# Performance work log

Hardware: AMD Instinct MI355X
Metric: run time of the kernel (lower is better)

Reference implementation:

```python
import jax, jax.numpy as jnp
import numpy as np

BN_EPS = 1e-3


def _knn_group(p1, p2, k):
    # p1, p2: [N, 3]. For each point in p1 find k nearest in p2.
    d2 = (jnp.sum(p1 * p1, -1)[:, None] + jnp.sum(p2 * p2, -1)[None, :]
          - 2.0 * (p1 @ p2.T))                      # [N, N]
    _, idx = jax.lax.top_k(-d2, k)                   # [N, k]
    nn = p2[idx]                                     # [N, k, 3]
    resi = nn - p1[:, None, :]                       # [N, k, 3]
    dist = jnp.linalg.norm(resi, axis=-1, keepdims=True)
    feat = jnp.concatenate([resi, dist], axis=-1)    # [N, k, 4]
    return feat, nn


def _conv_bn_relu(x, W, b, g, be):
    # x: [B, Cin, N, K]; 1x1 conv == channel matmul, BN uses batch stats (train mode)
    y = jnp.einsum('oi,binK->bonK', W, x) + b[None, :, None, None]
    m = jnp.mean(y, axis=(0, 2, 3), keepdims=True)
    v = jnp.var(y, axis=(0, 2, 3), keepdims=True)
    y = g[None, :, None, None] * (y - m) * jax.lax.rsqrt(v + BN_EPS) + be[None, :, None, None]
    return jax.nn.relu(y)


def setup_inputs() -> dict:
    key = jax.random.key(0)
    ks = jax.random.split(key, 8)
    B, N, k = 4, 4096, 32
    C = [4, 64, 64, 128]
    inp = {
        'points1': jax.random.normal(ks[0], (B, 3, N), jnp.float32),
        'points2': jax.random.normal(ks[1], (B, 3, N), jnp.float32),
        'k': k,
        't': jax.random.uniform(ks[2], (B,), jnp.float32),
    }
    for i in range(3):
        kw = jax.random.fold_in(ks[3], i)
        inp[f'W{i+1}'] = jax.random.normal(kw, (C[i + 1], C[i]), jnp.float32) * (1.0 / np.sqrt(C[i]))
        inp[f'b{i+1}'] = jnp.zeros((C[i + 1],), jnp.float32)
        inp[f'g{i+1}'] = jnp.ones((C[i + 1],), jnp.float32)
        inp[f'be{i+1}'] = jnp.zeros((C[i + 1],), jnp.float32)
    return inp


def reference(points1, points2, k, t, W1, b1, g1, be1, W2, b2, g2, be2, W3, b3, g3, be3):
    p1 = jnp.transpose(points1, (0, 2, 1))           # [B, N, 3]
    p2 = jnp.transpose(points2, (0, 2, 1))
    knn = jax.vmap(_knn_group, in_axes=(0, 0, None))
    f1, nn1 = knn(p1, p1, k)                          # [B, N, k, 4], [B, N, k, 3]
    f2, nn2 = knn(p1, p2, k)
    feats = jnp.concatenate([f1, f2], axis=2)         # [B, N, 2k, 4]
    grouped = jnp.concatenate([nn1, nn2], axis=2)     # [B, N, 2k, 3]
    x = jnp.transpose(feats, (0, 3, 1, 2))            # [B, 4, N, 2k]
    x = _conv_bn_relu(x, W1, b1, g1, be1)
    x = _conv_bn_relu(x, W2, b2, g2, be2)
    x = _conv_bn_relu(x, W3, b3, g3, be3)             # [B, 128, N, 2k]
    scores = jnp.max(x, axis=1)                       # [B, N, 2k]
    w = jax.nn.softmax(scores, axis=-1)               # [B, N, 2k]
    fused = jnp.einsum('bnk,bnkc->bcn', w, grouped)   # [B, 3, N]
    return fused
```

## Files before the change

kernel.cpp:

```cpp
#include <hip/hip_runtime.h>
#include <hip/hip_bf16.h>

#define B_   4
#define N_   4096
#define KNN_ 32
#define KK_  64
#define MTOT 1048576
#define BN_EPS 1e-3f

typedef unsigned int u32;
typedef unsigned long long u64;
typedef __attribute__((ext_vector_type(8))) short bf16x8;
typedef __attribute__((ext_vector_type(4))) float f32x4;

__device__ __forceinline__ ushort f2bf_bits(float f) {
    u32 b = __float_as_uint(f);
    b += 0x7fffu + ((b >> 16) & 1u);
    return (ushort)(b >> 16);
}

__device__ __forceinline__ float med3f(float a, float b, float c) {
    return __builtin_amdgcn_fmed3f(a, b, c);
}

__device__ __forceinline__ float rank_e3(float cx, float cy, float2 zw,
                                         float m2x, float m2y, float m2z) {
    return fmaf(m2x, cx, fmaf(m2y, cy, fmaf(m2z, zw.x, zw.y)));
}

__device__ __forceinline__ u32 ordkey(float f) {
    u32 u = __float_as_uint(f);
    return u ^ (u32)(((int)u >> 31) | 0x80000000);
}
__device__ __forceinline__ float ordinv(u32 k) {
    u32 u = (k & 0x80000000u) ? (k ^ 0x80000000u) : ~k;
    return __uint_as_float(u);
}

__global__ __launch_bounds__(512, 2) void knn_kernel(
    const float* __restrict__ p1, const float* __restrict__ p2,
    float* __restrict__ feats, float* __restrict__ mom)
{
    __shared__ float2 cxy[N_];
    __shared__ float2 czw[N_];

    const int tid  = threadIdx.x;
    const int wave = tid >> 6, lane = tid & 63;
    const int pb    = blockIdx.x >> 6;
    const int chunk = blockIdx.x & 63;
    const int pr = pb >> 2, b = pb & 3;
    const int start = chunk * 64;

    const float* srcb = (pr ? p2 : p1) + (size_t)b * 3 * N_;
    for (int n = tid; n < N_; n += 512) {
        float x = srcb[n], y = srcb[N_ + n], z = srcb[2*N_ + n];
        cxy[n] = make_float2(x, y);
        czw[n] = make_float2(z, fmaf(x, x, fmaf(y, y, z * z)));
    }
    __syncthreads();

    const float* p1b = p1 + (size_t)b * 3 * N_;
    const u64 below = (1ull << lane) - 1ull;
    const float FMAX = 3.402823466e+38f;

    for (int n = start + wave; n < start + 64; n += 8) {
        float qx, qy, qz;
        if (pr == 0) { float2 q = cxy[n]; qx = q.x; qy = q.y; qz = czw[n].x; }
        else         { qx = p1b[n]; qy = p1b[N_ + n]; qz = p1b[2*N_ + n]; }
        const float m2x = -2.0f * qx, m2y = -2.0f * qy, m2z = -2.0f * qz;

        float keys[64];
        float A0 = FMAX, A1 = FMAX, A2 = FMAX, A3 = FMAX;
        float B0 = FMAX, B1 = FMAX, B2 = FMAX, B3 = FMAX;
        #pragma unroll
        for (int j = 0; j < 32; ++j) {
            {
                float2 c  = cxy[j * 64 + lane];
                float2 zw = czw[j * 64 + lane];
                float  e  = rank_e3(c.x, c.y, zw, m2x, m2y, m2z);
                keys[j] = e;
                A3 = med3f(e, A2, A3);
                A2 = med3f(e, A1, A2);
                A1 = med3f(e, A0, A1);
                A0 = fminf(A0, e);
            }
            {
                float2 c  = cxy[(j + 32) * 64 + lane];
                float2 zw = czw[(j + 32) * 64 + lane];
                float  e  = rank_e3(c.x, c.y, zw, m2x, m2y, m2z);
                keys[j + 32] = e;
                B3 = med3f(e, B2, B3);
                B2 = med3f(e, B1, B2);
                B1 = med3f(e, B0, B1);
                B0 = fminf(B0, e);
            }
        }
        #pragma unroll
        for (int m = 0; m < 4; ++m) {
            float x = (m == 0) ? B0 : (m == 1) ? B1 : (m == 2) ? B2 : B3;
            A3 = med3f(x, A2, A3);
            A2 = med3f(x, A1, A2);
            A1 = med3f(x, A0, A1);
            A0 = fminf(A0, x);
        }
        u32 k0 = ordkey(A0), k1 = ordkey(A1), k2 = ordkey(A2), k3 = ordkey(A3);

        u32 mn = k0, mx = k3;
        #pragma unroll
        for (int off = 1; off < 64; off <<= 1) {
            mn = min(mn, (u32)__shfl_xor((int)mn, off, 64));
            mx = max(mx, (u32)__shfl_xor((int)mx, off, 64));
        }
        u32 lo = mn, hi = mx;
        while (lo < hi) {
            u32 mid = lo + ((hi - lo) >> 1);
            int c = __popcll(__ballot(k0 <= mid)) + __popcll(__ballot(k1 <= mid))
                  + __popcll(__ballot(k2 <= mid)) + __popcll(__ballot(k3 <= mid));
            if (c >= 32) hi = mid; else lo = mid + 1;
        }
        u32 T = lo;
        float Tf = ordinv(T);

        int nl;
        if (__ballot(A3 <= Tf) == 0ull) {
            nl = __popcll(__ballot(A0 < Tf)) + __popcll(__ballot(A1 < Tf))
               + __popcll(__ballot(A2 < Tf)) + __popcll(__ballot(A3 < Tf));
        } else {
            nl = 0;
            #pragma unroll
            for (int j = 0; j < 64; ++j) nl += __popcll(__ballot(keys[j] < Tf));
            if (nl > 31) {
                u32 lo2 = 0u, hi2 = T;
                while (lo2 < hi2) {
                    u32 mid = lo2 + ((hi2 - lo2) >> 1);
                    float mf = ordinv(mid);
                    int c = 0;
                    #pragma unroll
                    for (int j = 0; j < 64; ++j) c += __popcll(__ballot(keys[j] <= mf));
                    if (c >= 32) hi2 = mid; else lo2 = mid + 1;
                }
                T = lo2;
                Tf = ordinv(T);
                nl = 0;
                #pragma unroll
                for (int j = 0; j < 64; ++j) nl += __popcll(__ballot(keys[j] < Tf));
            }
        }
        const int need_eq = 32 - nl;

        float* fout = feats + ((size_t)(b * N_ + n) * KK_ + pr * KNN_) * 4;
        int base = 0, eq_seen = 0;
        #pragma unroll
        for (int j = 0; j < 64; ++j) {
            float e = keys[j];
            bool lt = e < Tf;
            bool eq = e == Tf;
            u64 mlt = __ballot(lt);
            u64 meq = __ballot(eq);
            if (mlt | meq) {
                int slot = -1;
                if (lt) slot = base + __popcll(mlt & below);
                else if (eq) {
                    int es = eq_seen + __popcll(meq & below);
                    if (es < need_eq) slot = nl + es;
                }
                if (slot >= 0) {
                    float2 c  = cxy[j * 64 + lane];
                    float2 zw = czw[j * 64 + lane];
                    float rx = c.x - qx, ry = c.y - qy, rz = zw.x - qz;
                    float dist = sqrtf(fmaf(rx, rx, fmaf(ry, ry, rz*rz)));
                    *(float4*)(fout + slot * 4) = make_float4(rx, ry, rz, dist);
                }
                base    += __popcll(mlt);
                eq_seen += __popcll(meq);
            }
        }
    }

    __syncthreads();
    float mm[14];
    #pragma unroll
    for (int s = 0; s < 14; ++s) mm[s] = 0.f;
    const float4* fb = (const float4*)feats
                     + ((size_t)(b * N_ + start) * KK_ + pr * KNN_);
    for (int idx = tid; idx < 64 * 32; idx += 512) {
        int row = idx >> 5, col = idx & 31;
        float4 f = fb[(size_t)row * KK_ + col];
        float rx = f.x, ry = f.y, rz = f.z, dist = f.w;
        mm[0] += rx; mm[1] += ry; mm[2] += rz; mm[3] += dist;
        mm[4]  = fmaf(rx, rx, mm[4]);   mm[5]  = fmaf(rx, ry, mm[5]);
        mm[6]  = fmaf(rx, rz, mm[6]);   mm[7]  = fmaf(rx, dist, mm[7]);
        mm[8]  = fmaf(ry, ry, mm[8]);   mm[9]  = fmaf(ry, rz, mm[9]);
        mm[10] = fmaf(ry, dist, mm[10]); mm[11] = fmaf(rz, rz, mm[11]);
        mm[12] = fmaf(rz, dist, mm[12]); mm[13] = fmaf(dist, dist, mm[13]);
    }
    #pragma unroll
    for (int s = 0; s < 14; ++s) {
        #pragma unroll
        for (int off = 1; off < 64; off <<= 1) mm[s] += __shfl_xor(mm[s], off, 64);
    }
    float* partf = (float*)cxy;
    if (lane == 0) {
        #pragma unroll
        for (int s = 0; s < 14; ++s) partf[wave * 14 + s] = mm[s];
    }
    __syncthreads();
    if (tid < 14) {
        float v = 0.f;
        #pragma unroll
        for (int w8 = 0; w8 < 8; ++w8) v += partf[w8 * 14 + tid];
        atomicAdd(&mom[tid * 16], v);
    }
}

__global__ __launch_bounds__(256) void conv2_mfma(
    const float* __restrict__ feats,
    const float* __restrict__ W1,
    const float* __restrict__ g1, const float* __restrict__ be1,
    const float* __restrict__ W2,
    const float* __restrict__ mom,
    ushort* __restrict__ y2F, float* __restrict__ s2S, float* __restrict__ s2Q)
{
    __shared__ float statS[64], statQ[64];
    const int tid = threadIdx.x;
    const int wid = tid >> 6, l = tid & 63, q = l >> 4, i = l & 15;
    if (tid < 64) { statS[tid] = 0.f; statQ[tid] = 0.f; }

    const float invM = 1.0f / MTOT;
    const float M0 = mom[0*16], M1 = mom[1*16], M2 = mom[2*16], M3 = mom[3*16];
    const float Sxx = mom[4*16],  Sxy = mom[5*16],  Sxz = mom[6*16],  Sxd = mom[7*16];
    const float Syy = mom[8*16],  Syz = mom[9*16],  Syd = mom[10*16];
    const float Szz = mom[11*16], Szd = mom[12*16], Sdd = mom[13*16];

    float4 w1f[16];
    float  c1v[16];
    #pragma unroll
    for (int h = 0; h < 2; ++h)
      #pragma unroll
      for (int j = 0; j < 8; ++j) {
        int ci = h*32 + q*8 + j;
        float w0 = W1[ci*4+0], w1 = W1[ci*4+1], w2 = W1[ci*4+2], w3 = W1[ci*4+3];
        float meanf = (w0*M0 + w1*M1 + w2*M2 + w3*M3) * invM;
        float qq = w0*(w0*Sxx + 2.f*(w1*Sxy + w2*Sxz + w3*Sxd))
                 + w1*(w1*Syy + 2.f*(w2*Syz + w3*Syd))
                 + w2*(w2*Szz + 2.f*w3*Szd)
                 + w3*w3*Sdd;
        float var = qq * invM - meanf * meanf;
        float sc  = g1[ci] * rsqrtf(var + BN_EPS);
        w1f[h*8+j] = make_float4(sc*w0, sc*w1, sc*w2, sc*w3);
        c1v[h*8+j] = fmaf(-sc, meanf, be1[ci]);
      }
    bf16x8 a2[4][2];
    #pragma unroll
    for (int t = 0; t < 4; ++t)
      #pragma unroll
      for (int h = 0; h < 2; ++h)
        #pragma unroll
        for (int j = 0; j < 8; ++j)
          a2[t][h][j] = (short)f2bf_bits(W2[(t*16 + i)*64 + h*32 + q*8 + j]);

    float ssum[16], ssq[16];
    #pragma unroll
    for (int s = 0; s < 16; ++s) { ssum[s] = 0.f; ssq[s] = 0.f; }
    __syncthreads();

    for (int r16 = 0; r16 < 16; ++r16) {
        const int row = blockIdx.x * 16 + r16;
        float4 f = ((const float4*)feats)[row*64 + wid*16 + i];
        bf16x8 xb[2];
        #pragma unroll
        for (int h = 0; h < 2; ++h)
          #pragma unroll
          for (int j = 0; j < 8; ++j) {
            float4 w = w1f[h*8+j];
            float x = fmaxf(fmaf(w.x, f.x, fmaf(w.y, f.y, fmaf(w.z, f.z, fmaf(w.w, f.w, c1v[h*8+j])))), 0.f);
            xb[h][j] = (short)f2bf_bits(x);
          }
        f32x4 acc[4];
        #pragma unroll
        for (int t = 0; t < 4; ++t) acc[t] = (f32x4){0.f,0.f,0.f,0.f};
        #pragma unroll
        for (int t = 0; t < 4; ++t) {
            acc[t] = __builtin_amdgcn_mfma_f32_16x16x32_bf16(a2[t][0], xb[0], acc[t], 0, 0, 0);
            acc[t] = __builtin_amdgcn_mfma_f32_16x16x32_bf16(a2[t][1], xb[1], acc[t], 0, 0, 0);
        }
        ushort* wp = y2F + row*4096 + wid*1024 + q*64 + i*4;
        #pragma unroll
        for (int t = 0; t < 4; ++t) {
            #pragma unroll
            for (int reg = 0; reg < 4; ++reg) {
                float y = acc[t][reg];
                ssum[t*4+reg] += y;
                ssq[t*4+reg]  = fmaf(y, y, ssq[t*4+reg]);
            }
            uint2 pk;
            pk.x = (u32)f2bf_bits(acc[t][0]) | ((u32)f2bf_bits(acc[t][1]) << 16);
            pk.y = (u32)f2bf_bits(acc[t][2]) | ((u32)f2bf_bits(acc[t][3]) << 16);
            *(uint2*)(wp + t*256) = pk;
        }
    }
    #pragma unroll
    for (int s = 0; s < 16; ++s) {
        #pragma unroll
        for (int off = 1; off < 16; off <<= 1) {
            ssum[s] += __shfl_xor(ssum[s], off, 64);
            ssq[s]  += __shfl_xor(ssq[s],  off, 64);
        }
    }
    if (i == 0) {
        #pragma unroll
        for (int s = 0; s < 16; ++s) {
            int co = (s >> 2)*16 + q*4 + (s & 3);
            atomicAdd(&statS[co], ssum[s]);
            atomicAdd(&statQ[co], ssq[s]);
        }
    }
    __syncthreads();
    if (tid < 64) { atomicAdd(&s2S[tid], statS[tid]); atomicAdd(&s2Q[tid], statQ[tid]); }
}

__global__ __launch_bounds__(256) void conv3_stats(
    ushort* __restrict__ y2F,
    const float* __restrict__ g2, const float* __restrict__ be2,
    const float* __restrict__ W3,
    const float* __restrict__ s2S, const float* __restrict__ s2Q,
    float* __restrict__ s3S, float* __restrict__ s3Q)
{
    __shared__ float statS[128], statQ[128];
    const int tid = threadIdx.x;
    const int w = tid >> 6, l = tid & 63, q = l >> 4, i = l & 15;
    const int ph = w >> 1, oh = w & 1;
    if (tid < 128) { statS[tid] = 0.f; statQ[tid] = 0.f; }

    float sc2v[16], sh2v[16];
    #pragma unroll
    for (int h = 0; h < 2; ++h)
      #pragma unroll
      for (int j = 0; j < 8; ++j) {
        int ci = h*32 + q*8 + j;
        float m  = s2S[ci] * (1.0f / MTOT);
        float v  = s2Q[ci] * (1.0f / MTOT) - m * m;
        float sc = g2[ci] * rsqrtf(v + BN_EPS);
        sc2v[h*8+j] = sc;
        sh2v[h*8+j] = fmaf(-sc, m, be2[ci]);
      }
    bf16x8 a3[4][2];
    #pragma unroll
    for (int t = 0; t < 4; ++t)
      #pragma unroll
      for (int h = 0; h < 2; ++h)
        #pragma unroll
        for (int j = 0; j < 8; ++j)
          a3[t][h][j] = (short)f2bf_bits(W3[((oh*4 + t)*16 + i)*64 + h*32 + q*8 + j]);

    float ssum[16], ssq[16];
    #pragma unroll
    for (int s = 0; s < 16; ++s) { ssum[s] = 0.f; ssq[s] = 0.f; }

    for (int r16 = 0; r16 < 16; ++r16) {
        const int row = blockIdx.x * 16 + r16;
        ushort* rp0 = y2F + row*4096 + (2*ph)*1024 + q*128 + i*4;
        ushort* rp1 = rp0 + 1024;
        uint2 a00 = *(const uint2*)(rp0);       uint2 a01 = *(const uint2*)(rp0 + 64);
        uint2 a10 = *(const uint2*)(rp0 + 512); uint2 a11 = *(const uint2*)(rp0 + 576);
        uint2 b00 = *(const uint2*)(rp1);       uint2 b01 = *(const uint2*)(rp1 + 64);
        uint2 b10 = *(const uint2*)(rp1 + 512); uint2 b11 = *(const uint2*)(rp1 + 576);

        bf16x8 xa[2], xc[2];
        #pragma unroll
        for (int pt2 = 0; pt2 < 2; ++pt2) {
            uint2 v00 = pt2 ? b00 : a00, v01 = pt2 ? b01 : a01;
            uint2 v10 = pt2 ? b10 : a10, v11 = pt2 ? b11 : a11;
            bf16x8* dst = pt2 ? xc : xa;
            #pragma unroll
            for (int h = 0; h < 2; ++h) {
                u32 w0 = h ? v10.x : v00.x, w1 = h ? v10.y : v00.y;
                u32 w2 = h ? v11.x : v01.x, w3 = h ? v11.y : v01.y;
                float xf[8];
                xf[0] = __uint_as_float(w0 << 16); xf[1] = __uint_as_float(w0 & 0xffff0000u);
                xf[2] = __uint_as_float(w1 << 16); xf[3] = __uint_as_float(w1 & 0xffff0000u);
                xf[4] = __uint_as_float(w2 << 16); xf[5] = __uint_as_float(w2 & 0xffff0000u);
                xf[6] = __uint_as_float(w3 << 16); xf[7] = __uint_as_float(w3 & 0xffff0000u);
                #pragma unroll
                for (int j = 0; j < 8; ++j) {
                    float x = fmaxf(fmaf(sc2v[h*8+j], xf[j], sh2v[h*8+j]), 0.f);
                    dst[h][j] = (short)f2bf_bits(x);
                }
            }
        }
        __syncthreads();
        if (oh == 0) {
            uint4 ua0 = *(uint4*)&xa[0], ua1 = *(uint4*)&xa[1];
            uint4 uc0 = *(uint4*)&xc[0], uc1 = *(uint4*)&xc[1];
            *(uint2*)(rp0)       = make_uint2(ua0.x, ua0.y);
            *(uint2*)(rp0 + 64)  = make_uint2(ua0.z, ua0.w);
            *(uint2*)(rp0 + 512) = make_uint2(ua1.x, ua1.y);
            *(uint2*)(rp0 + 576) = make_uint2(ua1.z, ua1.w);
            *(uint2*)(rp1)       = make_uint2(uc0.x, uc0.y);
            *(uint2*)(rp1 + 64)  = make_uint2(uc0.z, uc0.w);
            *(uint2*)(rp1 + 512) = make_uint2(uc1.x, uc1.y);
            *(uint2*)(rp1 + 576) = make_uint2(uc1.z, uc1.w);
        }
        #pragma unroll
        for (int t = 0; t < 4; ++t) {
            f32x4 A = (f32x4){0.f,0.f,0.f,0.f};
            A = __builtin_amdgcn_mfma_f32_16x16x32_bf16(a3[t][0], xa[0], A, 0, 0, 0);
            A = __builtin_amdgcn_mfma_f32_16x16x32_bf16(a3[t][1], xa[1], A, 0, 0, 0);
            f32x4 Bv = (f32x4){0.f,0.f,0.f,0.f};
            Bv = __builtin_amdgcn_mfma_f32_16x16x32_bf16(a3[t][0], xc[0], Bv, 0, 0, 0);
            Bv = __builtin_amdgcn_mfma_f32_16x16x32_bf16(a3[t][1], xc[1], Bv, 0, 0, 0);
            #pragma unroll
            for (int reg = 0; reg < 4; ++reg) {
                float ya = A[reg], yb = Bv[reg];
                ssum[t*4+reg] += ya + yb;
                ssq[t*4+reg]  = fmaf(ya, ya, fmaf(yb, yb, ssq[t*4+reg]));
            }
        }
    }
    #pragma unroll
    for (int s = 0; s < 16; ++s) {
        #pragma unroll
        for (int off = 1; off < 16; off <<= 1) {
            ssum[s] += __shfl_xor(ssum[s], off, 64);
            ssq[s]  += __shfl_xor(ssq[s],  off, 64);
        }
    }
    if (i == 0) {
        #pragma unroll
        for (int s = 0; s < 16; ++s) {
            int co = oh*64 + (s >> 2)*16 + q*4 + (s & 3);
            atomicAdd(&statS[co], ssum[s]);
            atomicAdd(&statQ[co], ssq[s]);
        }
    }
    __syncthreads();
    if (tid < 128) { atomicAdd(&s3S[tid], statS[tid]); atomicAdd(&s3Q[tid], statQ[tid]); }
}

__global__ __launch_bounds__(256) void conv3_final(
    const ushort* __restrict__ x3F,
    const float* __restrict__ W3,
    const float* __restrict__ g3, const float* __restrict__ be3,
    const float* __restrict__ s3S, const float* __restrict__ s3Q,
    const float4* __restrict__ feats4, const float* __restrict__ p1,
    float* __restrict__ outp)
{
    __shared__ float sc3L[128], sh3L[128];
    __shared__ float s2L[2][2][64];
    const int tid = threadIdx.x;
    const int w = tid >> 6, l = tid & 63, q = l >> 4, i = l & 15;
    const int ph = w >> 1, oh = w & 1;

    if (tid < 128) {
        float m  = s3S[tid] * (1.0f / MTOT);
        float v  = s3Q[tid] * (1.0f / MTOT) - m * m;
        float sc = g3[tid] * rsqrtf(v + BN_EPS);
        sc3L[tid] = sc;
        sh3L[tid] = fmaf(-sc, m, be3[tid]);
    }
    bf16x8 a3[4][2];
    #pragma unroll
    for (int t = 0; t < 4; ++t)
      #pragma unroll
      for (int h = 0; h < 2; ++h)
        #pragma unroll
        for (int j = 0; j < 8; ++j)
          a3[t][h][j] = (short)f2bf_bits(W3[((oh*4 + t)*16 + i)*64 + h*32 + q*8 + j]);
    __syncthreads();

    for (int r16 = 0; r16 < 16; ++r16) {
        const int row = blockIdx.x * 16 + r16;
        #pragma unroll
        for (int pt2 = 0; pt2 < 2; ++pt2) {
            const int pt = 2*ph + pt2;
            const ushort* rp = x3F + row*4096 + pt*1024 + q*128 + i*4;
            uint2 u00 = *(const uint2*)(rp);       uint2 u01 = *(const uint2*)(rp + 64);
            uint2 u10 = *(const uint2*)(rp + 512); uint2 u11 = *(const uint2*)(rp + 576);
            uint4 v0 = make_uint4(u00.x, u00.y, u01.x, u01.y);
            uint4 v1 = make_uint4(u10.x, u10.y, u11.x, u11.y);
            bf16x8 xb0 = *(bf16x8*)&v0, xb1 = *(bf16x8*)&v1;
            float mx = -3.4e38f;
            #pragma unroll
            for (int t = 0; t < 4; ++t) {
                f32x4 a = (f32x4){0.f,0.f,0.f,0.f};
                a = __builtin_amdgcn_mfma_f32_16x16x32_bf16(a3[t][0], xb0, a, 0, 0, 0);
                a = __builtin_amdgcn_mfma_f32_16x16x32_bf16(a3[t][1], xb1, a, 0, 0, 0);
                const int co = oh*64 + t*16 + q*4;
                float4 s4 = *(const float4*)&sc3L[co];
                float4 h4 = *(const float4*)&sh3L[co];
                mx = fmaxf(mx, fmaf(s4.x, a[0], h4.x));
                mx = fmaxf(mx, fmaf(s4.y, a[1], h4.y));
                mx = fmaxf(mx, fmaf(s4.z, a[2], h4.z));
                mx = fmaxf(mx, fmaf(s4.w, a[3], h4.w));
            }
            mx = fmaxf(mx, __shfl_xor(mx, 16, 64));
            mx = fmaxf(mx, __shfl_xor(mx, 32, 64));
            if (q == 0) s2L[r16 & 1][oh][pt*16 + i] = mx;
        }
        __syncthreads();
        if (w == 0) {
            float sc = fmaxf(fmaxf(s2L[r16 & 1][0][l], s2L[r16 & 1][1][l]), 0.f);
            float m2 = sc;
            #pragma unroll
            for (int off = 1; off < 64; off <<= 1) m2 = fmaxf(m2, __shfl_xor(m2, off, 64));
            float e = __expf(sc - m2);
            float se = e;
            #pragma unroll
            for (int off = 1; off < 64; off <<= 1) se += __shfl_xor(se, off, 64);
            float wgt = e / se;
            const int bb = row >> 12, n = row & 4095;
            float qx = p1[(size_t)bb*3*N_ + n];
            float qy = p1[(size_t)bb*3*N_ + N_ + n];
            float qz = p1[(size_t)bb*3*N_ + 2*N_ + n];
            float4 f4 = feats4[row*64 + l];
            float ox = wgt * (f4.x + qx), oy = wgt * (f4.y + qy), oz = wgt * (f4.z + qz);
            #pragma unroll
            for (int off = 1; off < 64; off <<= 1) {
                ox += __shfl_xor(ox, off, 64);
                oy += __shfl_xor(oy, off, 64);
                oz += __shfl_xor(oz, off, 64);
            }
            if (l == 0) {
                outp[bb*3*N_ + 0*N_ + n] = ox;
                outp[bb*3*N_ + 1*N_ + n] = oy;
                outp[bb*3*N_ + 2*N_ + n] = oz;
            }
        }
    }
}

extern "C" void kernel_launch(void* const* d_in, const int* in_sizes, int n_in,
                              void* d_out, int out_size, void* d_ws, size_t ws_size,
                              hipStream_t stream)
{
    const float* p1  = (const float*)d_in[0];
    const float* p2  = (const float*)d_in[1];
    const float* W1  = (const float*)d_in[4];
    const float* g1  = (const float*)d_in[6];
    const float* be1 = (const float*)d_in[7];
    const float* W2  = (const float*)d_in[8];
    const float* g2  = (const float*)d_in[10];
    const float* be2 = (const float*)d_in[11];
    const float* W3  = (const float*)d_in[12];
    const float* g3  = (const float*)d_in[14];
    const float* be3 = (const float*)d_in[15];

    char* ws = (char*)d_ws;
    const size_t OFF_FEATS = 4096;
    const size_t OFF_Y2    = OFF_FEATS + (size_t)MTOT * 4 * 4;
    const size_t NEEDED    = OFF_Y2 + (size_t)MTOT * 64 * 2;
    if (ws_size < NEEDED) return;

    float* s2S = (float*)(ws + 512);  float* s2Q = (float*)(ws + 768);
    float* s3S = (float*)(ws + 1024); float* s3Q = (float*)(ws + 1536);
    float* mom = (float*)(ws + 2048);
    float* feats = (float*)(ws + OFF_FEATS);
    ushort* y2F  = (ushort*)(ws + OFF_Y2);

    hipMemsetAsync(ws, 0, 4096, stream);

    knn_kernel<<<512, 512, 0, stream>>>(p1, p2, feats, mom);
    conv2_mfma<<<1024, 256, 0, stream>>>(feats, W1, g1, be1, W2, mom,
                                         y2F, s2S, s2Q);
    conv3_stats<<<1024, 256, 0, stream>>>(y2F, g2, be2, W3,
                                          s2S, s2Q, s3S, s3Q);
    conv3_final<<<1024, 256, 0, stream>>>(y2F, W3, g3, be3, s3S, s3Q,
                                          (const float4*)feats, p1,
                                          (float*)d_out);
}
```

Baseline: 419.9 us.

## Recompute conv1/conv2 activations per pass instead of materializing y2 in global memory

Removes the 128 MB bf16 y2 intermediate buffer. Each of the conv3 stats and final kernels now recomputes conv1 and conv2 from the 16-byte feats rows and stages the BN2-ReLU output in shared memory, where it feeds the conv3 MFMAs. This trades a global write plus two reads (and an in-place rewrite) for extra MFMA and VALU work and more barriers per row.

```diff
diff --git a/kernel.cpp b/kernel.cpp
--- a/kernel.cpp
+++ b/kernel.cpp
@@ -213,13 +213,13 @@
     }
 }
 
-__global__ __launch_bounds__(256) void conv2_mfma(
+__global__ __launch_bounds__(256) void conv2_stats(
     const float* __restrict__ feats,
     const float* __restrict__ W1,
     const float* __restrict__ g1, const float* __restrict__ be1,
     const float* __restrict__ W2,
     const float* __restrict__ mom,
-    ushort* __restrict__ y2F, float* __restrict__ s2S, float* __restrict__ s2Q)
+    float* __restrict__ s2S, float* __restrict__ s2Q)
 {
     __shared__ float statS[64], statQ[64];
     const int tid = threadIdx.x;
@@ -284,20 +284,14 @@
             acc[t] = __builtin_amdgcn_mfma_f32_16x16x32_bf16(a2[t][0], xb[0], acc[t], 0, 0, 0);
             acc[t] = __builtin_amdgcn_mfma_f32_16x16x32_bf16(a2[t][1], xb[1], acc[t], 0, 0, 0);
         }
-        ushort* wp = y2F + row*4096 + wid*1024 + q*64 + i*4;
-        #pragma unroll
-        for (int t = 0; t < 4; ++t) {
-            #pragma unroll
-            for (int reg = 0; reg < 4; ++reg) {
-                float y = acc[t][reg];
-                ssum[t*4+reg] += y;
-                ssq[t*4+reg]  = fmaf(y, y, ssq[t*4+reg]);
-            }
-            uint2 pk;
-            pk.x = (u32)f2bf_bits(acc[t][0]) | ((u32)f2bf_bits(acc[t][1]) << 16);
-            pk.y = (u32)f2bf_bits(acc[t][2]) | ((u32)f2bf_bits(acc[t][3]) << 16);
-            *(uint2*)(wp + t*256) = pk;
-        }
+        #pragma unroll
+        for (int t = 0; t < 4; ++t)
+          #pragma unroll
+          for (int reg = 0; reg < 4; ++reg) {
+            float y = acc[t][reg];
+            ssum[t*4+reg] += y;
+            ssq[t*4+reg]  = fmaf(y, y, ssq[t*4+reg]);
+          }
     }
     #pragma unroll
     for (int s = 0; s < 16; ++s) {
@@ -319,96 +313,126 @@
     if (tid < 64) { atomicAdd(&s2S[tid], statS[tid]); atomicAdd(&s2Q[tid], statQ[tid]); }
 }
 
-__global__ __launch_bounds__(256) void conv3_stats(
-    ushort* __restrict__ y2F,
+
+__global__ __launch_bounds__(256) void conv3_stats_f(
+    const float* __restrict__ feats,
+    const float* __restrict__ W1,
+    const float* __restrict__ g1, const float* __restrict__ be1,
+    const float* __restrict__ W2,
+    const float* __restrict__ mom,
     const float* __restrict__ g2, const float* __restrict__ be2,
     const float* __restrict__ W3,
     const float* __restrict__ s2S, const float* __restrict__ s2Q,
     float* __restrict__ s3S, float* __restrict__ s3Q)
 {
-    __shared__ float statS[128], statQ[128];
+    __shared__ ushort x3L[4096];
+    __shared__ float  statS[128], statQ[128];
+    __shared__ float4 w1L[64];
+    __shared__ float  c1L[64], sc2L[64], sh2L[64];
+
     const int tid = threadIdx.x;
     const int w = tid >> 6, l = tid & 63, q = l >> 4, i = l & 15;
-    const int ph = w >> 1, oh = w & 1;
+    const int ph = w >> 1, oh = w & 1, wid = w;
     if (tid < 128) { statS[tid] = 0.f; statQ[tid] = 0.f; }
 
-    float sc2v[16], sh2v[16];
-    #pragma unroll
-    for (int h = 0; h < 2; ++h)
-      #pragma unroll
-      for (int j = 0; j < 8; ++j) {
-        int ci = h*32 + q*8 + j;
-        float m  = s2S[ci] * (1.0f / MTOT);
-        float v  = s2Q[ci] * (1.0f / MTOT) - m * m;
-        float sc = g2[ci] * rsqrtf(v + BN_EPS);
-        sc2v[h*8+j] = sc;
-        sh2v[h*8+j] = fmaf(-sc, m, be2[ci]);
-      }
-    bf16x8 a3[4][2];
+    if (tid < 64) {
+        const int ci = tid;
+        const float invM = 1.0f / MTOT;
+        float M0 = mom[0*16], M1 = mom[1*16], M2 = mom[2*16], M3 = mom[3*16];
+        float Sxx = mom[4*16],  Sxy = mom[5*16],  Sxz = mom[6*16],  Sxd = mom[7*16];
+        float Syy = mom[8*16],  Syz = mom[9*16],  Syd = mom[10*16];
+        float Szz = mom[11*16], Szd = mom[12*16], Sdd = mom[13*16];
+        float w0 = W1[ci*4+0], w1 = W1[ci*4+1], w2 = W1[ci*4+2], w3 = W1[ci*4+3];
+        float meanf = (w0*M0 + w1*M1 + w2*M2 + w3*M3) * invM;
+        float qq = w0*(w0*Sxx + 2.f*(w1*Sxy + w2*Sxz + w3*Sxd))
+                 + w1*(w1*Syy + 2.f*(w2*Syz + w3*Syd))
+                 + w2*(w2*Szz + 2.f*w3*Szd)
+                 + w3*w3*Sdd;
+        float var = qq * invM - meanf * meanf;
+        float sc  = g1[ci] * rsqrtf(var + BN_EPS);
+        w1L[ci] = make_float4(sc*w0, sc*w1, sc*w2, sc*w3);
+        c1L[ci] = fmaf(-sc, meanf, be1[ci]);
+        float m2  = s2S[ci] * invM;
+        float v2  = s2Q[ci] * invM - m2 * m2;
+        float sc2 = g2[ci] * rsqrtf(v2 + BN_EPS);
+        sc2L[ci] = sc2;
+        sh2L[ci] = fmaf(-sc2, m2, be2[ci]);
+    }
+
+    bf16x8 a2[4][2], a3[4][2];
     #pragma unroll
     for (int t = 0; t < 4; ++t)
       #pragma unroll
       for (int h = 0; h < 2; ++h)
         #pragma unroll
-        for (int j = 0; j < 8; ++j)
+        for (int j = 0; j < 8; ++j) {
+          a2[t][h][j] = (short)f2bf_bits(W2[(t*16 + i)*64 + h*32 + q*8 + j]);
           a3[t][h][j] = (short)f2bf_bits(W3[((oh*4 + t)*16 + i)*64 + h*32 + q*8 + j]);
+        }
 
     float ssum[16], ssq[16];
     #pragma unroll
     for (int s = 0; s < 16; ++s) { ssum[s] = 0.f; ssq[s] = 0.f; }
+    __syncthreads();
 
     for (int r16 = 0; r16 < 16; ++r16) {
         const int row = blockIdx.x * 16 + r16;
-        ushort* rp0 = y2F + row*4096 + (2*ph)*1024 + q*128 + i*4;
-        ushort* rp1 = rp0 + 1024;
+        float4 f = ((const float4*)feats)[row*64 + wid*16 + i];
+        bf16x8 xb[2];
+        #pragma unroll
+        for (int h = 0; h < 2; ++h)
+          #pragma unroll
+          for (int j = 0; j < 8; ++j) {
+            float4 wv = w1L[h*32 + q*8 + j];
+            float c1 = c1L[h*32 + q*8 + j];
+            float x = fmaxf(fmaf(wv.x, f.x, fmaf(wv.y, f.y, fmaf(wv.z, f.z, fmaf(wv.w, f.w, c1)))), 0.f);
+            xb[h][j] = (short)f2bf_bits(x);
+          }
+        f32x4 acc[4];
+        #pragma unroll
+        for (int t = 0; t < 4; ++t) acc[t] = (f32x4){0.f,0.f,0.f,0.f};
+        #pragma unroll
+        for (int t = 0; t < 4; ++t) {
+            acc[t] = __builtin_amdgcn_mfma_f32_16x16x32_bf16(a2[t][0], xb[0], acc[t], 0, 0, 0);
+            acc[t] = __builtin_amdgcn_mfma_f32_16x16x32_bf16(a2[t][1], xb[1], acc[t], 0, 0, 0);
+        }
+        #pragma unroll
+        for (int t = 0; t < 4; ++t) {
+            ushort o[4];
+            #pragma unroll
+            for (int reg = 0; reg < 4; ++reg) {
+                ushort yb = f2bf_bits(acc[t][reg]);
+                float xf = __uint_as_float(((u32)yb) << 16);
+                float x3 = fmaxf(fmaf(sc2L[t*16 + q*4 + reg], xf, sh2L[t*16 + q*4 + reg]), 0.f);
+                o[reg] = f2bf_bits(x3);
+            }
+            uint2 pk;
+            pk.x = (u32)o[0] | ((u32)o[1] << 16);
+            pk.y = (u32)o[2] | ((u32)o[3] << 16);
+            *(uint2*)&x3L[wid*1024 + t*256 + q*64 + i*4] = pk;
+        }
+        __syncthreads();
+
+        const ushort* rp0 = x3L + (2*ph)*1024 + q*128 + i*4;
+        const ushort* rp1 = rp0 + 1024;
         uint2 a00 = *(const uint2*)(rp0);       uint2 a01 = *(const uint2*)(rp0 + 64);
         uint2 a10 = *(const uint2*)(rp0 + 512); uint2 a11 = *(const uint2*)(rp0 + 576);
         uint2 b00 = *(const uint2*)(rp1);       uint2 b01 = *(const uint2*)(rp1 + 64);
         uint2 b10 = *(const uint2*)(rp1 + 512); uint2 b11 = *(const uint2*)(rp1 + 576);
-
-        bf16x8 xa[2], xc[2];
-        #pragma unroll
-        for (int pt2 = 0; pt2 < 2; ++pt2) {
-            uint2 v00 = pt2 ? b00 : a00, v01 = pt2 ? b01 : a01;
-            uint2 v10 = pt2 ? b10 : a10, v11 = pt2 ? b11 : a11;
-            bf16x8* dst = pt2 ? xc : xa;
-            #pragma unroll
-            for (int h = 0; h < 2; ++h) {
-                u32 w0 = h ? v10.x : v00.x, w1 = h ? v10.y : v00.y;
-                u32 w2 = h ? v11.x : v01.x, w3 = h ? v11.y : v01.y;
-                float xf[8];
-                xf[0] = __uint_as_float(w0 << 16); xf[1] = __uint_as_float(w0 & 0xffff0000u);
-                xf[2] = __uint_as_float(w1 << 16); xf[3] = __uint_as_float(w1 & 0xffff0000u);
-                xf[4] = __uint_as_float(w2 << 16); xf[5] = __uint_as_float(w2 & 0xffff0000u);
-                xf[6] = __uint_as_float(w3 << 16); xf[7] = __uint_as_float(w3 & 0xffff0000u);
-                #pragma unroll
-                for (int j = 0; j < 8; ++j) {
-                    float x = fmaxf(fmaf(sc2v[h*8+j], xf[j], sh2v[h*8+j]), 0.f);
-                    dst[h][j] = (short)f2bf_bits(x);
-                }
-            }
-        }
-        __syncthreads();
-        if (oh == 0) {
-            uint4 ua0 = *(uint4*)&xa[0], ua1 = *(uint4*)&xa[1];
-            uint4 uc0 = *(uint4*)&xc[0], uc1 = *(uint4*)&xc[1];
-            *(uint2*)(rp0)       = make_uint2(ua0.x, ua0.y);
-            *(uint2*)(rp0 + 64)  = make_uint2(ua0.z, ua0.w);
-            *(uint2*)(rp0 + 512) = make_uint2(ua1.x, ua1.y);
-            *(uint2*)(rp0 + 576) = make_uint2(ua1.z, ua1.w);
-            *(uint2*)(rp1)       = make_uint2(uc0.x, uc0.y);
-            *(uint2*)(rp1 + 64)  = make_uint2(uc0.z, uc0.w);
-            *(uint2*)(rp1 + 512) = make_uint2(uc1.x, uc1.y);
-            *(uint2*)(rp1 + 576) = make_uint2(uc1.z, uc1.w);
-        }
+        uint4 va0 = make_uint4(a00.x, a00.y, a01.x, a01.y);
+        uint4 va1 = make_uint4(a10.x, a10.y, a11.x, a11.y);
+        uint4 vc0 = make_uint4(b00.x, b00.y, b01.x, b01.y);
+        uint4 vc1 = make_uint4(b10.x, b10.y, b11.x, b11.y);
+        bf16x8 xa0 = *(bf16x8*)&va0, xa1 = *(bf16x8*)&va1;
+        bf16x8 xc0 = *(bf16x8*)&vc0, xc1 = *(bf16x8*)&vc1;
         #pragma unroll
         for (int t = 0; t < 4; ++t) {
             f32x4 A = (f32x4){0.f,0.f,0.f,0.f};
-            A = __builtin_amdgcn_mfma_f32_16x16x32_bf16(a3[t][0], xa[0], A, 0, 0, 0);
-            A = __builtin_amdgcn_mfma_f32_16x16x32_bf16(a3[t][1], xa[1], A, 0, 0, 0);
+            A = __builtin_amdgcn_mfma_f32_16x16x32_bf16(a3[t][0], xa0, A, 0, 0, 0);
+            A = __builtin_amdgcn_mfma_f32_16x16x32_bf16(a3[t][1], xa1, A, 0, 0, 0);
             f32x4 Bv = (f32x4){0.f,0.f,0.f,0.f};
-            Bv = __builtin_amdgcn_mfma_f32_16x16x32_bf16(a3[t][0], xc[0], Bv, 0, 0, 0);
-            Bv = __builtin_amdgcn_mfma_f32_16x16x32_bf16(a3[t][1], xc[1], Bv, 0, 0, 0);
+            Bv = __builtin_amdgcn_mfma_f32_16x16x32_bf16(a3[t][0], xc0, Bv, 0, 0, 0);
+            Bv = __builtin_amdgcn_mfma_f32_16x16x32_bf16(a3[t][1], xc1, Bv, 0, 0, 0);
             #pragma unroll
             for (int reg = 0; reg < 4; ++reg) {
                 float ya = A[reg], yb = Bv[reg];
@@ -416,6 +440,7 @@
                 ssq[t*4+reg]  = fmaf(ya, ya, fmaf(yb, yb, ssq[t*4+reg]));
             }
         }
+        __syncthreads();
     }
     #pragma unroll
     for (int s = 0; s < 16; ++s) {
@@ -437,43 +462,115 @@
     if (tid < 128) { atomicAdd(&s3S[tid], statS[tid]); atomicAdd(&s3Q[tid], statQ[tid]); }
 }
 
-__global__ __launch_bounds__(256) void conv3_final(
-    const ushort* __restrict__ x3F,
+__global__ __launch_bounds__(256) void conv3_final_f(
+    const float* __restrict__ feats,
+    const float* __restrict__ W1,
+    const float* __restrict__ g1, const float* __restrict__ be1,
+    const float* __restrict__ W2,
+    const float* __restrict__ mom,
+    const float* __restrict__ g2, const float* __restrict__ be2,
     const float* __restrict__ W3,
+    const float* __restrict__ s2S, const float* __restrict__ s2Q,
     const float* __restrict__ g3, const float* __restrict__ be3,
     const float* __restrict__ s3S, const float* __restrict__ s3Q,
-    const float4* __restrict__ feats4, const float* __restrict__ p1,
-    float* __restrict__ outp)
+    const float* __restrict__ p1, float* __restrict__ outp)
 {
-    __shared__ float sc3L[128], sh3L[128];
-    __shared__ float s2L[2][2][64];
+    __shared__ ushort x3L[4096];
+    __shared__ float4 w1L[64];
+    __shared__ float  c1L[64], sc2L[64], sh2L[64];
+    __shared__ float  sc3L[128], sh3L[128];
+    __shared__ float  s2L[2][2][64];
+
     const int tid = threadIdx.x;
     const int w = tid >> 6, l = tid & 63, q = l >> 4, i = l & 15;
-    const int ph = w >> 1, oh = w & 1;
-
+    const int ph = w >> 1, oh = w & 1, wid = w;
+
+    if (tid < 64) {
+        const int ci = tid;
+        const float invM = 1.0f / MTOT;
+        float M0 = mom[0*16], M1 = mom[1*16], M2 = mom[2*16], M3 = mom[3*16];
+        float Sxx = mom[4*16],  Sxy = mom[5*16],  Sxz = mom[6*16],  Sxd = mom[7*16];
+        float Syy = mom[8*16],  Syz = mom[9*16],  Syd = mom[10*16];
+        float Szz = mom[11*16], Szd = mom[12*16], Sdd = mom[13*16];
+        float w0 = W1[ci*4+0], w1 = W1[ci*4+1], w2 = W1[ci*4+2], w3 = W1[ci*4+3];
+        float meanf = (w0*M0 + w1*M1 + w2*M2 + w3*M3) * invM;
+        float qq = w0*(w0*Sxx + 2.f*(w1*Sxy + w2*Sxz + w3*Sxd))
+                 + w1*(w1*Syy + 2.f*(w2*Syz + w3*Syd))
+                 + w2*(w2*Szz + 2.f*w3*Szd)
+                 + w3*w3*Sdd;
+        float var = qq * invM - meanf * meanf;
+        float sc  = g1[ci] * rsqrtf(var + BN_EPS);
+        w1L[ci] = make_float4(sc*w0, sc*w1, sc*w2, sc*w3);
+        c1L[ci] = fmaf(-sc, meanf, be1[ci]);
+        float m2  = s2S[ci] * invM;
+        float v2  = s2Q[ci] * invM - m2 * m2;
+        float sc2 = g2[ci] * rsqrtf(v2 + BN_EPS);
+        sc2L[ci] = sc2;
+        sh2L[ci] = fmaf(-sc2, m2, be2[ci]);
+    }
     if (tid < 128) {
-        float m  = s3S[tid] * (1.0f / MTOT);
-        float v  = s3Q[tid] * (1.0f / MTOT) - m * m;
+        const float invM = 1.0f / MTOT;
+        float m  = s3S[tid] * invM;
+        float v  = s3Q[tid] * invM - m * m;
         float sc = g3[tid] * rsqrtf(v + BN_EPS);
         sc3L[tid] = sc;
         sh3L[tid] = fmaf(-sc, m, be3[tid]);
     }
-    bf16x8 a3[4][2];
+
+    bf16x8 a2[4][2], a3[4][2];
     #pragma unroll
     for (int t = 0; t < 4; ++t)
       #pragma unroll
       for (int h = 0; h < 2; ++h)
         #pragma unroll
-        for (int j = 0; j < 8; ++j)
+        for (int j = 0; j < 8; ++j) {
+          a2[t][h][j] = (short)f2bf_bits(W2[(t*16 + i)*64 + h*32 + q*8 + j]);
           a3[t][h][j] = (short)f2bf_bits(W3[((oh*4 + t)*16 + i)*64 + h*32 + q*8 + j]);
+        }
     __syncthreads();
 
     for (int r16 = 0; r16 < 16; ++r16) {
         const int row = blockIdx.x * 16 + r16;
+        float4 f = ((const float4*)feats)[row*64 + wid*16 + i];
+        bf16x8 xb[2];
+        #pragma unroll
+        for (int h = 0; h < 2; ++h)
+          #pragma unroll
+          for (int j = 0; j < 8; ++j) {
+            float4 wv = w1L[h*32 + q*8 + j];
+            float c1 = c1L[h*32 + q*8 + j];
+            float x = fmaxf(fmaf(wv.x, f.x, fmaf(wv.y, f.y, fmaf(wv.z, f.z, fmaf(wv.w, f.w, c1)))), 0.f);
+            xb[h][j] = (short)f2bf_bits(x);
+          }
+        f32x4 acc[4];
+        #pragma unroll
+        for (int t = 0; t < 4; ++t) acc[t] = (f32x4){0.f,0.f,0.f,0.f};
+        #pragma unroll
+        for (int t = 0; t < 4; ++t) {
+            acc[t] = __builtin_amdgcn_mfma_f32_16x16x32_bf16(a2[t][0], xb[0], acc[t], 0, 0, 0);
+            acc[t] = __builtin_amdgcn_mfma_f32_16x16x32_bf16(a2[t][1], xb[1], acc[t], 0, 0, 0);
+        }
+        #pragma unroll
+        for (int t = 0; t < 4; ++t) {
+            ushort o[4];
+            #pragma unroll
+            for (int reg = 0; reg < 4; ++reg) {
+                ushort yb = f2bf_bits(acc[t][reg]);
+                float xf = __uint_as_float(((u32)yb) << 16);
+                float x3 = fmaxf(fmaf(sc2L[t*16 + q*4 + reg], xf, sh2L[t*16 + q*4 + reg]), 0.f);
+                o[reg] = f2bf_bits(x3);
+            }
+            uint2 pk;
+            pk.x = (u32)o[0] | ((u32)o[1] << 16);
+            pk.y = (u32)o[2] | ((u32)o[3] << 16);
+            *(uint2*)&x3L[wid*1024 + t*256 + q*64 + i*4] = pk;
+        }
+        __syncthreads();
+
         #pragma unroll
         for (int pt2 = 0; pt2 < 2; ++pt2) {
             const int pt = 2*ph + pt2;
-            const ushort* rp = x3F + row*4096 + pt*1024 + q*128 + i*4;
+            const ushort* rp = x3L + pt*1024 + q*128 + i*4;
             uint2 u00 = *(const uint2*)(rp);       uint2 u01 = *(const uint2*)(rp + 64);
             uint2 u10 = *(const uint2*)(rp + 512); uint2 u11 = *(const uint2*)(rp + 576);
             uint4 v0 = make_uint4(u00.x, u00.y, u01.x, u01.y);
@@ -498,6 +595,7 @@
             if (q == 0) s2L[r16 & 1][oh][pt*16 + i] = mx;
         }
         __syncthreads();
+
         if (w == 0) {
             float sc = fmaxf(fmaxf(s2L[r16 & 1][0][l], s2L[r16 & 1][1][l]), 0.f);
             float m2 = sc;
@@ -512,7 +610,7 @@
             float qx = p1[(size_t)bb*3*N_ + n];
             float qy = p1[(size_t)bb*3*N_ + N_ + n];
             float qz = p1[(size_t)bb*3*N_ + 2*N_ + n];
-            float4 f4 = feats4[row*64 + l];
+            float4 f4 = ((const float4*)feats)[row*64 + l];
             float ox = wgt * (f4.x + qx), oy = wgt * (f4.y + qy), oz = wgt * (f4.z + qz);
             #pragma unroll
             for (int off = 1; off < 64; off <<= 1) {
@@ -547,24 +645,22 @@
 
     char* ws = (char*)d_ws;
     const size_t OFF_FEATS = 4096;
-    const size_t OFF_Y2    = OFF_FEATS + (size_t)MTOT * 4 * 4;
-    const size_t NEEDED    = OFF_Y2 + (size_t)MTOT * 64 * 2;
+    const size_t NEEDED    = OFF_FEATS + (size_t)MTOT * 4 * 4;
     if (ws_size < NEEDED) return;
 
     float* s2S = (float*)(ws + 512);  float* s2Q = (float*)(ws + 768);
     float* s3S = (float*)(ws + 1024); float* s3Q = (float*)(ws + 1536);
     float* mom = (float*)(ws + 2048);
     float* feats = (float*)(ws + OFF_FEATS);
-    ushort* y2F  = (ushort*)(ws + OFF_Y2);
 
     hipMemsetAsync(ws, 0, 4096, stream);
 
     knn_kernel<<<512, 512, 0, stream>>>(p1, p2, feats, mom);
-    conv2_mfma<<<1024, 256, 0, stream>>>(feats, W1, g1, be1, W2, mom,
-                                         y2F, s2S, s2Q);
-    conv3_stats<<<1024, 256, 0, stream>>>(y2F, g2, be2, W3,
-                                          s2S, s2Q, s3S, s3Q);
-    conv3_final<<<1024, 256, 0, stream>>>(y2F, W3, g3, be3, s3S, s3Q,
-                                          (const float4*)feats, p1,
-                                          (float*)d_out);
-}
+    conv2_stats<<<1024, 256, 0, stream>>>(feats, W1, g1, be1, W2, mom, s2S, s2Q);
+    conv3_stats_f<<<1024, 256, 0, stream>>>(feats, W1, g1, be1, W2, mom,
+                                            g2, be2, W3, s2S, s2Q, s3S, s3Q);
+    conv3_final_f<<<1024, 256, 0, stream>>>(feats, W1, g1, be1, W2, mom,
+                                            g2, be2, W3, s2S, s2Q,
+                                            g3, be3, s3S, s3Q, p1,
+                                            (float*)d_out);
+}
```

Measured after the change: 499.2 us. 18.9% more time.

## Repartition conv3_stats so each wave owns one point-chunk and all 128 outputs

Applied to the files above, without the earlier changes.

Each wave in conv3_stats previously covered two point-chunks and half of the output channels. That duplicated the y2 load, BN and bf16 conversion across the two output-half waves, and needed a per-row __syncthreads before the in-place write-back. Now each wave loads and normalizes one distinct chunk, writes it back without a barrier, and runs MFMAs for all 128 output channels. The BN2 scale/shift is computed once into shared memory instead of per-thread registers. The trade-off is higher register pressure: the W3 fragments and stat accumulators double, which may lower occupancy or cause spills.

```diff
diff --git a/kernel.cpp b/kernel.cpp
--- a/kernel.cpp
+++ b/kernel.cpp
@@ -327,98 +327,77 @@
     float* __restrict__ s3S, float* __restrict__ s3Q)
 {
     __shared__ float statS[128], statQ[128];
+    __shared__ float sc2L[64], sh2L[64];
     const int tid = threadIdx.x;
     const int w = tid >> 6, l = tid & 63, q = l >> 4, i = l & 15;
-    const int ph = w >> 1, oh = w & 1;
     if (tid < 128) { statS[tid] = 0.f; statQ[tid] = 0.f; }
-
-    float sc2v[16], sh2v[16];
-    #pragma unroll
-    for (int h = 0; h < 2; ++h)
-      #pragma unroll
-      for (int j = 0; j < 8; ++j) {
-        int ci = h*32 + q*8 + j;
-        float m  = s2S[ci] * (1.0f / MTOT);
-        float v  = s2Q[ci] * (1.0f / MTOT) - m * m;
-        float sc = g2[ci] * rsqrtf(v + BN_EPS);
-        sc2v[h*8+j] = sc;
-        sh2v[h*8+j] = fmaf(-sc, m, be2[ci]);
-      }
-    bf16x8 a3[4][2];
-    #pragma unroll
-    for (int t = 0; t < 4; ++t)
+    if (tid < 64) {
+        float m  = s2S[tid] * (1.0f / MTOT);
+        float v  = s2Q[tid] * (1.0f / MTOT) - m * m;
+        float sc = g2[tid] * rsqrtf(v + BN_EPS);
+        sc2L[tid] = sc;
+        sh2L[tid] = fmaf(-sc, m, be2[tid]);
+    }
+
+    bf16x8 a3[8][2];
+    #pragma unroll
+    for (int t8 = 0; t8 < 8; ++t8)
       #pragma unroll
       for (int h = 0; h < 2; ++h)
         #pragma unroll
         for (int j = 0; j < 8; ++j)
-          a3[t][h][j] = (short)f2bf_bits(W3[((oh*4 + t)*16 + i)*64 + h*32 + q*8 + j]);
-
-    float ssum[16], ssq[16];
-    #pragma unroll
-    for (int s = 0; s < 16; ++s) { ssum[s] = 0.f; ssq[s] = 0.f; }
+          a3[t8][h][j] = (short)f2bf_bits(W3[(t8*16 + i)*64 + h*32 + q*8 + j]);
+
+    float ssum[32], ssq[32];
+    #pragma unroll
+    for (int s = 0; s < 32; ++s) { ssum[s] = 0.f; ssq[s] = 0.f; }
+    __syncthreads();
 
     for (int r16 = 0; r16 < 16; ++r16) {
         const int row = blockIdx.x * 16 + r16;
-        ushort* rp0 = y2F + row*4096 + (2*ph)*1024 + q*128 + i*4;
-        ushort* rp1 = rp0 + 1024;
-        uint2 a00 = *(const uint2*)(rp0);       uint2 a01 = *(const uint2*)(rp0 + 64);
-        uint2 a10 = *(const uint2*)(rp0 + 512); uint2 a11 = *(const uint2*)(rp0 + 576);
-        uint2 b00 = *(const uint2*)(rp1);       uint2 b01 = *(const uint2*)(rp1 + 64);
-        uint2 b10 = *(const uint2*)(rp1 + 512); uint2 b11 = *(const uint2*)(rp1 + 576);
-
-        bf16x8 xa[2], xc[2];
-        #pragma unroll
-        for (int pt2 = 0; pt2 < 2; ++pt2) {
-            uint2 v00 = pt2 ? b00 : a00, v01 = pt2 ? b01 : a01;
-            uint2 v10 = pt2 ? b10 : a10, v11 = pt2 ? b11 : a11;
-            bf16x8* dst = pt2 ? xc : xa;
-            #pragma unroll
-            for (int h = 0; h < 2; ++h) {
-                u32 w0 = h ? v10.x : v00.x, w1 = h ? v10.y : v00.y;
-                u32 w2 = h ? v11.x : v01.x, w3 = h ? v11.y : v01.y;
-                float xf[8];
-                xf[0] = __uint_as_float(w0 << 16); xf[1] = __uint_as_float(w0 & 0xffff0000u);
-                xf[2] = __uint_as_float(w1 << 16); xf[3] = __uint_as_float(w1 & 0xffff0000u);
-                xf[4] = __uint_as_float(w2 << 16); xf[5] = __uint_as_float(w2 & 0xffff0000u);
-                xf[6] = __uint_as_float(w3 << 16); xf[7] = __uint_as_float(w3 & 0xffff0000u);
-                #pragma unroll
-                for (int j = 0; j < 8; ++j) {
-                    float x = fmaxf(fmaf(sc2v[h*8+j], xf[j], sh2v[h*8+j]), 0.f);
-                    dst[h][j] = (short)f2bf_bits(x);
-                }
-            }
-        }
-        __syncthreads();
-        if (oh == 0) {
-            uint4 ua0 = *(uint4*)&xa[0], ua1 = *(uint4*)&xa[1];
-            uint4 uc0 = *(uint4*)&xc[0], uc1 = *(uint4*)&xc[1];
-            *(uint2*)(rp0)       = make_uint2(ua0.x, ua0.y);
-            *(uint2*)(rp0 + 64)  = make_uint2(ua0.z, ua0.w);
-            *(uint2*)(rp0 + 512) = make_uint2(ua1.x, ua1.y);
-            *(uint2*)(rp0 + 576) = make_uint2(ua1.z, ua1.w);
-            *(uint2*)(rp1)       = make_uint2(uc0.x, uc0.y);
-            *(uint2*)(rp1 + 64)  = make_uint2(uc0.z, uc0.w);
-            *(uint2*)(rp1 + 512) = make_uint2(uc1.x, uc1.y);
-            *(uint2*)(rp1 + 576) = make_uint2(uc1.z, uc1.w);
-        }
-        #pragma unroll
-        for (int t = 0; t < 4; ++t) {
+        ushort* rp = y2F + row*4096 + w*1024 + q*128 + i*4;
+        uint2 u00 = *(const uint2*)(rp);
+        uint2 u01 = *(const uint2*)(rp + 64);
+        uint2 u10 = *(const uint2*)(rp + 512);
+        uint2 u11 = *(const uint2*)(rp + 576);
+
+        bf16x8 xb[2];
+        #pragma unroll
+        for (int h = 0; h < 2; ++h) {
+            u32 w0 = h ? u10.x : u00.x, w1 = h ? u10.y : u00.y;
+            u32 w2 = h ? u11.x : u01.x, w3 = h ? u11.y : u01.y;
+            float xf[8];
+            xf[0] = __uint_as_float(w0 << 16); xf[1] = __uint_as_float(w0 & 0xffff0000u);
+            xf[2] = __uint_as_float(w1 << 16); xf[3] = __uint_as_float(w1 & 0xffff0000u);
+            xf[4] = __uint_as_float(w2 << 16); xf[5] = __uint_as_float(w2 & 0xffff0000u);
+            xf[6] = __uint_as_float(w3 << 16); xf[7] = __uint_as_float(w3 & 0xffff0000u);
+            #pragma unroll
+            for (int j = 0; j < 8; ++j) {
+                float x = fmaxf(fmaf(sc2L[h*32 + q*8 + j], xf[j], sh2L[h*32 + q*8 + j]), 0.f);
+                xb[h][j] = (short)f2bf_bits(x);
+            }
+        }
+        uint4 ub0 = *(uint4*)&xb[0], ub1 = *(uint4*)&xb[1];
+        *(uint2*)(rp)       = make_uint2(ub0.x, ub0.y);
+        *(uint2*)(rp + 64)  = make_uint2(ub0.z, ub0.w);
+        *(uint2*)(rp + 512) = make_uint2(ub1.x, ub1.y);
+        *(uint2*)(rp + 576) = make_uint2(ub1.z, ub1.w);
+
+        #pragma unroll
+        for (int t8 = 0; t8 < 8; ++t8) {
             f32x4 A = (f32x4){0.f,0.f,0.f,0.f};
-            A = __builtin_amdgcn_mfma_f32_16x16x32_bf16(a3[t][0], xa[0], A, 0, 0, 0);
-            A = __builtin_amdgcn_mfma_f32_16x16x32_bf16(a3[t][1], xa[1], A, 0, 0, 0);
-            f32x4 Bv = (f32x4){0.f,0.f,0.f,0.f};
-            Bv = __builtin_amdgcn_mfma_f32_16x16x32_bf16(a3[t][0], xc[0], Bv, 0, 0, 0);
-            Bv = __builtin_amdgcn_mfma_f32_16x16x32_bf16(a3[t][1], xc[1], Bv, 0, 0, 0);
+            A = __builtin_amdgcn_mfma_f32_16x16x32_bf16(a3[t8][0], xb[0], A, 0, 0, 0);
+            A = __builtin_amdgcn_mfma_f32_16x16x32_bf16(a3[t8][1], xb[1], A, 0, 0, 0);
             #pragma unroll
             for (int reg = 0; reg < 4; ++reg) {
-                float ya = A[reg], yb = Bv[reg];
-                ssum[t*4+reg] += ya + yb;
-                ssq[t*4+reg]  = fmaf(ya, ya, fmaf(yb, yb, ssq[t*4+reg]));
-            }
-        }
-    }
-    #pragma unroll
-    for (int s = 0; s < 16; ++s) {
+                float y = A[reg];
+                ssum[t8*4+reg] += y;
+                ssq[t8*4+reg]  = fmaf(y, y, ssq[t8*4+reg]);
+            }
+        }
+    }
+    #pragma unroll
+    for (int s = 0; s < 32; ++s) {
         #pragma unroll
         for (int off = 1; off < 16; off <<= 1) {
             ssum[s] += __shfl_xor(ssum[s], off, 64);
@@ -427,8 +406,8 @@
     }
     if (i == 0) {
         #pragma unroll
-        for (int s = 0; s < 16; ++s) {
-            int co = oh*64 + (s >> 2)*16 + q*4 + (s & 3);
+        for (int s = 0; s < 32; ++s) {
+            int co = (s >> 2)*16 + q*4 + (s & 3);
             atomicAdd(&statS[co], ssum[s]);
             atomicAdd(&statQ[co], ssq[s]);
         }
```

Measured after the change: 436.6 us. 1.04x slower.
